# Optimization experiments

Measured on AMD Instinct MI355X. Metric: run time of the kernel, lower is better.

The kernel has to match this reference:

```python
import jax, jax.numpy as jnp
import numpy as np

N_NODES = 100000


def gcn_conv(x, edge_index, W, b, n_nodes):
    """PyG GCNConv: linear -> add self-loops -> symmetric-normalized scatter-sum -> bias."""
    h = x @ W  # [N, F_out]
    loop = jnp.arange(n_nodes, dtype=edge_index.dtype)
    src = jnp.concatenate([edge_index[0], loop])
    dst = jnp.concatenate([edge_index[1], loop])
    # degree of destination nodes (self-loops included)
    deg = jax.ops.segment_sum(jnp.ones_like(dst, dtype=h.dtype), dst, num_segments=n_nodes)
    dinv = jnp.where(deg > 0, jax.lax.rsqrt(deg), 0.0)
    norm = dinv[src] * dinv[dst]  # [E+N]
    msg = h[src] * norm[:, None]  # gather + scale
    out = jax.ops.segment_sum(msg, dst, num_segments=n_nodes)  # scatter-add
    return out + b


def setup_inputs() -> dict:
    key = jax.random.key(0)
    k1, k2, k3, k4 = jax.random.split(key, 4)
    d_in, hidden, out = 128, 256, 64
    x = jax.random.normal(k1, (N_NODES, d_in), dtype=jnp.float32)
    edge_index = jax.random.randint(k2, (2, 800000), 0, N_NODES, dtype=jnp.int64)
    W1 = jax.random.normal(k3, (d_in, hidden), dtype=jnp.float32) * (1.0 / np.sqrt(d_in))
    b1 = jnp.zeros((hidden,), dtype=jnp.float32)
    W2 = jax.random.normal(k4, (hidden, out), dtype=jnp.float32) * (1.0 / np.sqrt(hidden))
    b2 = jnp.zeros((out,), dtype=jnp.float32)
    return {"x": x, "edge_index": edge_index, "W1": W1, "b1": b1, "W2": W2, "b2": b2}


def reference(x, edge_index, W1, b1, W2, b2):
    h = jax.nn.relu(gcn_conv(x, edge_index, W1, b1, N_NODES))
    # dropout p=0 (module default) -> identity
    return gcn_conv(h, edge_index, W2, b2, N_NODES)
```

## Files before the change

kernel.cpp:

```cpp
#include <hip/hip_runtime.h>
#include <hip/hip_bf16.h>

#define N_NODES 100000
#define D_IN 128
#define HID 256
#define D_OUT 64
#define TR 32
#define NBUK 196
#define BSH 9
#define MGRID 625

typedef __attribute__((ext_vector_type(8))) short bf8;
typedef __attribute__((ext_vector_type(4))) float f4;

static __device__ __forceinline__ unsigned short f2bf(float f) {
    __hip_bfloat16 h = __float2bfloat16(f);
    return *reinterpret_cast<unsigned short*>(&h);
}
static __device__ __forceinline__ float bflo(unsigned int u) { return __uint_as_float(u << 16); }
static __device__ __forceinline__ float bfhi(unsigned int u) { return __uint_as_float(u & 0xffff0000u); }

static __device__ __forceinline__ void fma8(float* a, float w, uint4 u) {
    a[0] += w * bflo(u.x); a[1] += w * bfhi(u.x);
    a[2] += w * bflo(u.y); a[3] += w * bfhi(u.y);
    a[4] += w * bflo(u.z); a[5] += w * bfhi(u.z);
    a[6] += w * bflo(u.w); a[7] += w * bfhi(u.w);
}
static __device__ __forceinline__ void fma4(float* a, float w, uint2 u) {
    a[0] += w * bflo(u.x); a[1] += w * bfhi(u.x);
    a[2] += w * bflo(u.y); a[3] += w * bfhi(u.y);
}


__global__ __launch_bounds__(256) void k_prep(const float* __restrict__ x,
                                              unsigned long long* __restrict__ xb,
                                              const float* __restrict__ W1,
                                              unsigned short* __restrict__ W1t,
                                              const float* __restrict__ W2,
                                              unsigned short* __restrict__ W2t,
                                              const int* __restrict__ dst, int E,
                                              int* __restrict__ hist2d) {
    int b = blockIdx.x, t = threadIdx.x;
    if (b < 12500) {
        int i = b * 256 + t;
        float4 v = ((const float4*)x)[i];
        unsigned long long o = (unsigned long long)f2bf(v.x) |
                               ((unsigned long long)f2bf(v.y) << 16) |
                               ((unsigned long long)f2bf(v.z) << 32) |
                               ((unsigned long long)f2bf(v.w) << 48);
        xb[i] = o;
    } else if (b < 12628) {
        int i = (b - 12500) * 256 + t;
        int n = i >> 7, k = i & 127;
        W1t[i] = f2bf(W1[k * HID + n]);
    } else if (b < 12692) {
        int i = (b - 12628) * 256 + t;
        int n = i >> 8, k = i & 255;
        W2t[i] = f2bf(W2[k * D_OUT + n]);
    } else {
        int hb = b - 12692;
        __shared__ int h[NBUK];
        if (t < NBUK) h[t] = 0;
        __syncthreads();
        int base = hb * 4096;
        for (int j = 0; j < 16; j++) {
            int e = base + j * 256 + t;
            if (e < E) atomicAdd(&h[dst[e] >> BSH], 1);
        }
        __syncthreads();
        if (t < NBUK) hist2d[hb * NBUK + t] = h[t];
    }
}


__global__ __launch_bounds__(256) void k_scanB1(const int* __restrict__ hist2d,
                                                int* __restrict__ blockbase,
                                                int* __restrict__ bsumB, int nbb) {
    __shared__ int s[256];
    int u = blockIdx.x, t = threadIdx.x;
    int v = (t < nbb) ? hist2d[t * NBUK + u] : 0;
    s[t] = v;
    __syncthreads();
    for (int off = 1; off < 256; off <<= 1) {
        int w = (t >= off) ? s[t - off] : 0;
        __syncthreads();
        s[t] += w;
        __syncthreads();
    }
    if (t < nbb) blockbase[t * NBUK + u] = s[t] - v;
    if (t == 255) bsumB[u] = s[255];
}

static __device__ __forceinline__ void bucket_scan(const int* __restrict__ bsumB,
                                                   int* s, int* exs, int t) {
    int v = (t < NBUK) ? bsumB[t] : 0;
    s[t] = v;
    __syncthreads();
    for (int off = 1; off < 256; off <<= 1) {
        int w = (t >= off) ? s[t - off] : 0;
        __syncthreads();
        s[t] += w;
        __syncthreads();
    }
    if (t < NBUK) exs[t] = s[t] - v;
    if (t == NBUK - 1) exs[NBUK] = s[t];
    __syncthreads();
}


__global__ __launch_bounds__(256) void k_bin(const int* __restrict__ src,
                                             const int* __restrict__ dst, int E,
                                             const int* __restrict__ blockbase,
                                             const int* __restrict__ bsumB,
                                             unsigned int* __restrict__ bin) {
    __shared__ int s[256], exs[NBUK + 1];
    __shared__ int baseL[NBUK], rankL[NBUK];
    int t = threadIdx.x;
    bucket_scan(bsumB, s, exs, t);
    if (t < NBUK) {
        baseL[t] = exs[t] + blockbase[blockIdx.x * NBUK + t];
        rankL[t] = 0;
    }
    __syncthreads();
    int base = blockIdx.x * 4096;
    for (int j = 0; j < 16; j++) {
        int e = base + j * 256 + t;
        if (e < E) {
            int sv = src[e], d = dst[e];
            int bu = d >> BSH;
            int r = atomicAdd(&rankL[bu], 1);
            bin[baseL[bu] + r] = ((unsigned int)(d & 511) << 17) | (unsigned int)sv;
        }
    }
}


__global__ __launch_bounds__(256) void k_cntscan(const unsigned int* __restrict__ bin,
                                                 const int* __restrict__ bsumB,
                                                 int* __restrict__ row_ptr,
                                                 float* __restrict__ dinv) {
    __shared__ int sb[256], exs[NBUK + 1];
    __shared__ int c[512];
    __shared__ int s[256];
    int b = blockIdx.x, t = threadIdx.x;
    bucket_scan(bsumB, sb, exs, t);
    int lo = exs[b], hi = exs[b + 1];
    c[t] = 0;
    c[t + 256] = 0;
    __syncthreads();
    for (int e = lo + t; e < hi; e += 256) atomicAdd(&c[bin[e] >> 17], 1);
    __syncthreads();
    int a0 = c[2 * t], a1 = c[2 * t + 1];
    s[t] = a0 + a1;
    __syncthreads();
    for (int off = 1; off < 256; off <<= 1) {
        int u = (t >= off) ? s[t - off] : 0;
        __syncthreads();
        s[t] += u;
        __syncthreads();
    }
    int ex = (t > 0) ? s[t - 1] : 0;
    int n0 = (b << BSH) + 2 * t;
    if (n0 < N_NODES) {
        row_ptr[n0] = lo + ex;
        dinv[n0] = rsqrtf((float)a0 + 1.0f);
    }
    if (n0 + 1 < N_NODES) {
        row_ptr[n0 + 1] = lo + ex + a0;
        dinv[n0 + 1] = rsqrtf((float)a1 + 1.0f);
    }
    if (b == NBUK - 1 && t == 255) row_ptr[N_NODES] = exs[NBUK];
}


__global__ __launch_bounds__(256) void k_place(const unsigned int* __restrict__ bin,
                                               const int* __restrict__ bsumB,
                                               const int* __restrict__ row_ptr,
                                               const float* __restrict__ dinv,
                                               int2* __restrict__ cw) {
    __shared__ int sb[256], exs[NBUK + 1];
    __shared__ int cur[512];
    __shared__ float dl[512];
    int b = blockIdx.x, t = threadIdx.x;
    bucket_scan(bsumB, sb, exs, t);
    int node0 = b << BSH;
    int nbn = N_NODES - node0;
    if (nbn > 512) nbn = 512;
    if (t < nbn) {
        cur[t] = row_ptr[node0 + t];
        dl[t] = dinv[node0 + t];
    }
    if (t + 256 < nbn) {
        cur[t + 256] = row_ptr[node0 + t + 256];
        dl[t + 256] = dinv[node0 + t + 256];
    }
    __syncthreads();
    int lo = exs[b], hi = exs[b + 1];
    for (int e = lo + t; e < hi; e += 256) {
        unsigned int rec = bin[e];
        int sv = rec & 0x1FFFF;
        int dloc = rec >> 17;
        int pos = atomicAdd(&cur[dloc], 1);
        int2 v;
        v.x = sv;
        v.y = __float_as_int(dinv[sv] * dl[dloc]);
        cw[pos] = v;
    }
}


__global__ __launch_bounds__(256) void k_pull1(const int* __restrict__ row_ptr,
                                               const int2* __restrict__ cw,
                                               const uint4* __restrict__ xb4,
                                               const float* __restrict__ dinv,
                                               uint4* __restrict__ agg4) {
    int wave = (blockIdx.x * 256 + threadIdx.x) >> 6;
    int lane = threadIdx.x & 63;
    int g = lane >> 4, l = lane & 15;
    int node = wave * 4 + g;
    int beg = row_ptr[node], end = row_ptr[node + 1];
    float di = dinv[node];
    float a[8] = {0, 0, 0, 0, 0, 0, 0, 0};
    fma8(a, di * di, xb4[(size_t)node * 16 + l]);
    int e = beg;
    if (e + 4 <= end) {
        int2 c0 = cw[e], c1 = cw[e + 1], c2 = cw[e + 2], c3 = cw[e + 3];
        uint4 u0 = xb4[(size_t)c0.x * 16 + l];
        uint4 u1 = xb4[(size_t)c1.x * 16 + l];
        uint4 u2 = xb4[(size_t)c2.x * 16 + l];
        uint4 u3 = xb4[(size_t)c3.x * 16 + l];
        e += 4;
        for (; e + 4 <= end; e += 4) {
            int2 d0 = cw[e], d1 = cw[e + 1], d2 = cw[e + 2], d3 = cw[e + 3];
            uint4 v0 = xb4[(size_t)d0.x * 16 + l];
            uint4 v1 = xb4[(size_t)d1.x * 16 + l];
            uint4 v2 = xb4[(size_t)d2.x * 16 + l];
            uint4 v3 = xb4[(size_t)d3.x * 16 + l];
            fma8(a, __int_as_float(c0.y), u0);
            fma8(a, __int_as_float(c1.y), u1);
            fma8(a, __int_as_float(c2.y), u2);
            fma8(a, __int_as_float(c3.y), u3);
            c0 = d0; c1 = d1; c2 = d2; c3 = d3;
            u0 = v0; u1 = v1; u2 = v2; u3 = v3;
        }
        fma8(a, __int_as_float(c0.y), u0);
        fma8(a, __int_as_float(c1.y), u1);
        fma8(a, __int_as_float(c2.y), u2);
        fma8(a, __int_as_float(c3.y), u3);
    }
    for (; e < end; e++) {
        int2 c = cw[e];
        fma8(a, __int_as_float(c.y), xb4[(size_t)c.x * 16 + l]);
    }
    uint4 o;
    o.x = (unsigned int)f2bf(a[0]) | ((unsigned int)f2bf(a[1]) << 16);
    o.y = (unsigned int)f2bf(a[2]) | ((unsigned int)f2bf(a[3]) << 16);
    o.z = (unsigned int)f2bf(a[4]) | ((unsigned int)f2bf(a[5]) << 16);
    o.w = (unsigned int)f2bf(a[6]) | ((unsigned int)f2bf(a[7]) << 16);
    agg4[(size_t)node * 16 + l] = o;
}


__global__ __launch_bounds__(256) void k_fused_mfma(unsigned short* __restrict__ agg,
                                                    const unsigned short* __restrict__ W1t,
                                                    const float* __restrict__ b1,
                                                    const unsigned short* __restrict__ W2t) {
    __shared__ char sH[TR * HID * 2];
    int t = threadIdx.x, wave = t >> 6, lane = t & 63;
    int lr = lane & 15, lg = lane >> 4;

    bf8 w1f[4][4];
#pragma unroll
    for (int kk = 0; kk < 4; kk++)
#pragma unroll
        for (int tt = 0; tt < 4; tt++)
            w1f[kk][tt] = *(const bf8*)(W1t + (size_t)(wave * 64 + tt * 16 + lr) * D_IN + kk * 32 + lg * 8);
    bf8 w2f[8];
#pragma unroll
    for (int kk = 0; kk < 8; kk++)
        w2f[kk] = *(const bf8*)(W2t + (size_t)(wave * 16 + lr) * HID + kk * 32 + lg * 8);
    float bias[4];
#pragma unroll
    for (int tt = 0; tt < 4; tt++) bias[tt] = b1[wave * 64 + tt * 16 + lr];

    for (int it = 0; it < 5; it++) {
        size_t row0 = ((size_t)blockIdx.x + (size_t)it * MGRID) * TR;

        f4 acc1[4][2];
#pragma unroll
        for (int tt = 0; tt < 4; tt++)
#pragma unroll
            for (int h = 0; h < 2; h++) acc1[tt][h] = (f4){0.f, 0.f, 0.f, 0.f};

#pragma unroll
        for (int kk = 0; kk < 4; kk++) {
            bf8 a0 = *(const bf8*)(agg + (row0 + lr) * 128 + kk * 32 + lg * 8);
            bf8 a1 = *(const bf8*)(agg + (row0 + 16 + lr) * 128 + kk * 32 + lg * 8);
#pragma unroll
            for (int tt = 0; tt < 4; tt++) {
                acc1[tt][0] = __builtin_amdgcn_mfma_f32_16x16x32_bf16(a0, w1f[kk][tt], acc1[tt][0], 0, 0, 0);
                acc1[tt][1] = __builtin_amdgcn_mfma_f32_16x16x32_bf16(a1, w1f[kk][tt], acc1[tt][1], 0, 0, 0);
            }
        }

#pragma unroll
        for (int tt = 0; tt < 4; tt++) {
            int colc = wave * 64 + tt * 16 + lr;
#pragma unroll
            for (int h = 0; h < 2; h++) {
#pragma unroll
                for (int ri = 0; ri < 4; ri++) {
                    int row = h * 16 + lg * 4 + ri;
                    float hv = acc1[tt][h][ri] + bias[tt];
                    hv = hv > 0.f ? hv : 0.f;
                    *(unsigned short*)(sH + ((row * 512 + colc * 2) ^ ((row & 7) << 4))) = f2bf(hv);
                }
            }
        }
        __syncthreads();

        f4 acc2[2];
        acc2[0] = (f4){0.f, 0.f, 0.f, 0.f};
        acc2[1] = (f4){0.f, 0.f, 0.f, 0.f};
#pragma unroll
        for (int kk = 0; kk < 8; kk++) {
            bf8 a0 = *(const bf8*)(sH + ((lr * 512 + kk * 64 + lg * 16) ^ ((lr & 7) << 4)));
            bf8 a1 = *(const bf8*)(sH + (((16 + lr) * 512 + kk * 64 + lg * 16) ^ (((16 + lr) & 7) << 4)));
            acc2[0] = __builtin_amdgcn_mfma_f32_16x16x32_bf16(a0, w2f[kk], acc2[0], 0, 0, 0);
            acc2[1] = __builtin_amdgcn_mfma_f32_16x16x32_bf16(a1, w2f[kk], acc2[1], 0, 0, 0);
        }
        int colc = wave * 16 + lr;
#pragma unroll
        for (int h = 0; h < 2; h++)
#pragma unroll
            for (int ri = 0; ri < 4; ri++) {
                int row = h * 16 + lg * 4 + ri;
                agg[(row0 + row) * 128 + colc] = f2bf(acc2[h][ri]);
            }
        __syncthreads();
    }
}


__global__ __launch_bounds__(256) void k_pull2(const int* __restrict__ row_ptr,
                                               const int2* __restrict__ cw,
                                               const uint2* __restrict__ m2,
                                               const float* __restrict__ dinv,
                                               const float* __restrict__ b2,
                                               float4* __restrict__ out4) {
    int wave = (blockIdx.x * 256 + threadIdx.x) >> 6;
    int lane = threadIdx.x & 63;
    int g = lane >> 4, l = lane & 15;
    int node = wave * 4 + g;
    int beg = row_ptr[node], end = row_ptr[node + 1];
    float di = dinv[node];
    float a[4] = {0, 0, 0, 0};
    fma4(a, di * di, m2[(size_t)node * 32 + l]);
    int e = beg;
    if (e + 4 <= end) {
        int2 c0 = cw[e], c1 = cw[e + 1], c2 = cw[e + 2], c3 = cw[e + 3];
        uint2 u0 = m2[(size_t)c0.x * 32 + l];
        uint2 u1 = m2[(size_t)c1.x * 32 + l];
        uint2 u2 = m2[(size_t)c2.x * 32 + l];
        uint2 u3 = m2[(size_t)c3.x * 32 + l];
        e += 4;
        for (; e + 4 <= end; e += 4) {
            int2 d0 = cw[e], d1 = cw[e + 1], d2 = cw[e + 2], d3 = cw[e + 3];
            uint2 v0 = m2[(size_t)d0.x * 32 + l];
            uint2 v1 = m2[(size_t)d1.x * 32 + l];
            uint2 v2 = m2[(size_t)d2.x * 32 + l];
            uint2 v3 = m2[(size_t)d3.x * 32 + l];
            fma4(a, __int_as_float(c0.y), u0);
            fma4(a, __int_as_float(c1.y), u1);
            fma4(a, __int_as_float(c2.y), u2);
            fma4(a, __int_as_float(c3.y), u3);
            c0 = d0; c1 = d1; c2 = d2; c3 = d3;
            u0 = v0; u1 = v1; u2 = v2; u3 = v3;
        }
        fma4(a, __int_as_float(c0.y), u0);
        fma4(a, __int_as_float(c1.y), u1);
        fma4(a, __int_as_float(c2.y), u2);
        fma4(a, __int_as_float(c3.y), u3);
    }
    for (; e < end; e++) {
        int2 c = cw[e];
        fma4(a, __int_as_float(c.y), m2[(size_t)c.x * 32 + l]);
    }
    float4 bv = ((const float4*)b2)[l];
    float4 o;
    o.x = a[0] + bv.x;
    o.y = a[1] + bv.y;
    o.z = a[2] + bv.z;
    o.w = a[3] + bv.w;
    out4[(size_t)node * 16 + l] = o;
}


extern "C" void kernel_launch(void* const* d_in, const int* in_sizes, int n_in,
                              void* d_out, int out_size, void* d_ws, size_t ws_size,
                              hipStream_t stream) {
    const float* x  = (const float*)d_in[0];
    const int*   ei = (const int*)d_in[1];
    const float* W1 = (const float*)d_in[2];
    const float* b1 = (const float*)d_in[3];
    const float* W2 = (const float*)d_in[4];
    const float* b2 = (const float*)d_in[5];
    float* out = (float*)d_out;

    const int E = in_sizes[1] / 2;
    const int* src = ei;
    const int* dst = ei + E;

    char* ws = (char*)d_ws;
    int* row_ptr        = (int*)(ws + 0);
    int2* cw            = (int2*)(ws + 400640);
    float* dinv         = (float*)(ws + 6800640);
    unsigned short* W1t = (unsigned short*)(ws + 7201024);
    unsigned short* W2t = (unsigned short*)(ws + 7266560);
    unsigned short* xb  = (unsigned short*)(ws + 7299328);
    unsigned short* aggb = (unsigned short*)(ws + 32899328);
    unsigned int* bin   = (unsigned int*)aggb;
    int* hist2d         = (int*)((char*)aggb + 3200256);
    int* blockbase      = (int*)((char*)aggb + 3354112);
    int* bsumB          = (int*)((char*)aggb + 3507968);

    const int NBB = (E + 4095) / 4096;

    k_prep<<<12692 + NBB, 256, 0, stream>>>(x, (unsigned long long*)xb, W1, W1t, W2, W2t,
                                            dst, E, hist2d);
    k_scanB1<<<NBUK, 256, 0, stream>>>(hist2d, blockbase, bsumB, NBB);
    k_bin<<<NBB, 256, 0, stream>>>(src, dst, E, blockbase, bsumB, bin);
    k_cntscan<<<NBUK, 256, 0, stream>>>(bin, bsumB, row_ptr, dinv);
    k_place<<<NBUK, 256, 0, stream>>>(bin, bsumB, row_ptr, dinv, cw);
    k_pull1<<<6250, 256, 0, stream>>>(row_ptr, cw, (const uint4*)xb, dinv, (uint4*)aggb);
    k_fused_mfma<<<MGRID, 256, 0, stream>>>(aggb, W1t, b1, W2t);
    k_pull2<<<6250, 256, 0, stream>>>(row_ptr, cw, (const uint2*)aggb, dinv, b2, (float4*)out);
}
```

Baseline: 149.6 us.

## Assign one wave per node in pull kernels, splitting edges across four slots

Result: slower. 162.1 us (+8.4%).

```diff
diff --git a/kernel.cpp b/kernel.cpp
--- a/kernel.cpp
+++ b/kernel.cpp
@@ -214,50 +214,47 @@
                                                const uint4* __restrict__ xb4,
                                                const float* __restrict__ dinv,
                                                uint4* __restrict__ agg4) {
-    int wave = (blockIdx.x * 256 + threadIdx.x) >> 6;
+    int node = (blockIdx.x * 256 + threadIdx.x) >> 6;
     int lane = threadIdx.x & 63;
-    int g = lane >> 4, l = lane & 15;
-    int node = wave * 4 + g;
+    int slot = lane >> 4, l = lane & 15;
     int beg = row_ptr[node], end = row_ptr[node + 1];
     float di = dinv[node];
     float a[8] = {0, 0, 0, 0, 0, 0, 0, 0};
-    fma8(a, di * di, xb4[(size_t)node * 16 + l]);
-    int e = beg;
-    if (e + 4 <= end) {
-        int2 c0 = cw[e], c1 = cw[e + 1], c2 = cw[e + 2], c3 = cw[e + 3];
-        uint4 u0 = xb4[(size_t)c0.x * 16 + l];
-        uint4 u1 = xb4[(size_t)c1.x * 16 + l];
-        uint4 u2 = xb4[(size_t)c2.x * 16 + l];
-        uint4 u3 = xb4[(size_t)c3.x * 16 + l];
-        e += 4;
-        for (; e + 4 <= end; e += 4) {
-            int2 d0 = cw[e], d1 = cw[e + 1], d2 = cw[e + 2], d3 = cw[e + 3];
-            uint4 v0 = xb4[(size_t)d0.x * 16 + l];
-            uint4 v1 = xb4[(size_t)d1.x * 16 + l];
-            uint4 v2 = xb4[(size_t)d2.x * 16 + l];
-            uint4 v3 = xb4[(size_t)d3.x * 16 + l];
-            fma8(a, __int_as_float(c0.y), u0);
-            fma8(a, __int_as_float(c1.y), u1);
-            fma8(a, __int_as_float(c2.y), u2);
-            fma8(a, __int_as_float(c3.y), u3);
-            c0 = d0; c1 = d1; c2 = d2; c3 = d3;
-            u0 = v0; u1 = v1; u2 = v2; u3 = v3;
-        }
-        fma8(a, __int_as_float(c0.y), u0);
-        fma8(a, __int_as_float(c1.y), u1);
-        fma8(a, __int_as_float(c2.y), u2);
-        fma8(a, __int_as_float(c3.y), u3);
-    }
-    for (; e < end; e++) {
-        int2 c = cw[e];
-        fma8(a, __int_as_float(c.y), xb4[(size_t)c.x * 16 + l]);
-    }
-    uint4 o;
-    o.x = (unsigned int)f2bf(a[0]) | ((unsigned int)f2bf(a[1]) << 16);
-    o.y = (unsigned int)f2bf(a[2]) | ((unsigned int)f2bf(a[3]) << 16);
-    o.z = (unsigned int)f2bf(a[4]) | ((unsigned int)f2bf(a[5]) << 16);
-    o.w = (unsigned int)f2bf(a[6]) | ((unsigned int)f2bf(a[7]) << 16);
-    agg4[(size_t)node * 16 + l] = o;
+    float ws = (slot == 0) ? di * di : 0.f;
+    fma8(a, ws, xb4[(size_t)node * 16 + l]);
+    int deg = end - beg;
+    if (deg > 0) {
+        int nb = (deg + 3) >> 2;
+        int e = beg + slot;
+        bool valid = e < end;
+        int2 c = cw[valid ? e : beg];
+        float w = valid ? __int_as_float(c.y) : 0.f;
+        uint4 u = xb4[(size_t)c.x * 16 + l];
+        for (int it = 1; it < nb; it++) {
+            e += 4;
+            bool v2 = e < end;
+            int2 c2 = cw[v2 ? e : beg];
+            float nw = v2 ? __int_as_float(c2.y) : 0.f;
+            uint4 nu = xb4[(size_t)c2.x * 16 + l];
+            fma8(a, w, u);
+            w = nw;
+            u = nu;
+        }
+        fma8(a, w, u);
+    }
+#pragma unroll
+    for (int i = 0; i < 8; i++) {
+        a[i] += __shfl_xor(a[i], 16);
+        a[i] += __shfl_xor(a[i], 32);
+    }
+    if (slot == 0) {
+        uint4 o;
+        o.x = (unsigned int)f2bf(a[0]) | ((unsigned int)f2bf(a[1]) << 16);
+        o.y = (unsigned int)f2bf(a[2]) | ((unsigned int)f2bf(a[3]) << 16);
+        o.z = (unsigned int)f2bf(a[4]) | ((unsigned int)f2bf(a[5]) << 16);
+        o.w = (unsigned int)f2bf(a[6]) | ((unsigned int)f2bf(a[7]) << 16);
+        agg4[(size_t)node * 16 + l] = o;
+    }
 }
 
 
@@ -348,51 +345,48 @@
                                                const float* __restrict__ dinv,
                                                const float* __restrict__ b2,
                                                float4* __restrict__ out4) {
-    int wave = (blockIdx.x * 256 + threadIdx.x) >> 6;
+    int node = (blockIdx.x * 256 + threadIdx.x) >> 6;
     int lane = threadIdx.x & 63;
-    int g = lane >> 4, l = lane & 15;
-    int node = wave * 4 + g;
+    int slot = lane >> 4, l = lane & 15;
     int beg = row_ptr[node], end = row_ptr[node + 1];
     float di = dinv[node];
     float a[4] = {0, 0, 0, 0};
-    fma4(a, di * di, m2[(size_t)node * 32 + l]);
-    int e = beg;
-    if (e + 4 <= end) {
-        int2 c0 = cw[e], c1 = cw[e + 1], c2 = cw[e + 2], c3 = cw[e + 3];
-        uint2 u0 = m2[(size_t)c0.x * 32 + l];
-        uint2 u1 = m2[(size_t)c1.x * 32 + l];
-        uint2 u2 = m2[(size_t)c2.x * 32 + l];
-        uint2 u3 = m2[(size_t)c3.x * 32 + l];
-        e += 4;
-        for (; e + 4 <= end; e += 4) {
-            int2 d0 = cw[e], d1 = cw[e + 1], d2 = cw[e + 2], d3 = cw[e + 3];
-            uint2 v0 = m2[(size_t)d0.x * 32 + l];
-            uint2 v1 = m2[(size_t)d1.x * 32 + l];
-            uint2 v2 = m2[(size_t)d2.x * 32 + l];
-            uint2 v3 = m2[(size_t)d3.x * 32 + l];
-            fma4(a, __int_as_float(c0.y), u0);
-            fma4(a, __int_as_float(c1.y), u1);
-            fma4(a, __int_as_float(c2.y), u2);
-            fma4(a, __int_as_float(c3.y), u3);
-            c0 = d0; c1 = d1; c2 = d2; c3 = d3;
-            u0 = v0; u1 = v1; u2 = v2; u3 = v3;
-        }
-        fma4(a, __int_as_float(c0.y), u0);
-        fma4(a, __int_as_float(c1.y), u1);
-        fma4(a, __int_as_float(c2.y), u2);
-        fma4(a, __int_as_float(c3.y), u3);
-    }
-    for (; e < end; e++) {
-        int2 c = cw[e];
-        fma4(a, __int_as_float(c.y), m2[(size_t)c.x * 32 + l]);
-    }
-    float4 bv = ((const float4*)b2)[l];
-    float4 o;
-    o.x = a[0] + bv.x;
-    o.y = a[1] + bv.y;
-    o.z = a[2] + bv.z;
-    o.w = a[3] + bv.w;
-    out4[(size_t)node * 16 + l] = o;
+    float ws = (slot == 0) ? di * di : 0.f;
+    fma4(a, ws, m2[(size_t)node * 32 + l]);
+    int deg = end - beg;
+    if (deg > 0) {
+        int nb = (deg + 3) >> 2;
+        int e = beg + slot;
+        bool valid = e < end;
+        int2 c = cw[valid ? e : beg];
+        float w = valid ? __int_as_float(c.y) : 0.f;
+        uint2 u = m2[(size_t)c.x * 32 + l];
+        for (int it = 1; it < nb; it++) {
+            e += 4;
+            bool v2 = e < end;
+            int2 c2 = cw[v2 ? e : beg];
+            float nw = v2 ? __int_as_float(c2.y) : 0.f;
+            uint2 nu = m2[(size_t)c2.x * 32 + l];
+            fma4(a, w, u);
+            w = nw;
+            u = nu;
+        }
+        fma4(a, w, u);
+    }
+#pragma unroll
+    for (int i = 0; i < 4; i++) {
+        a[i] += __shfl_xor(a[i], 16);
+        a[i] += __shfl_xor(a[i], 32);
+    }
+    if (slot == 0) {
+        float4 bv = ((const float4*)b2)[l];
+        float4 o;
+        o.x = a[0] + bv.x;
+        o.y = a[1] + bv.y;
+        o.z = a[2] + bv.z;
+        o.w = a[3] + bv.w;
+        out4[(size_t)node * 16 + l] = o;
+    }
 }
 
 
@@ -432,7 +426,7 @@
     k_bin<<<NBB, 256, 0, stream>>>(src, dst, E, blockbase, bsumB, bin);
     k_cntscan<<<NBUK, 256, 0, stream>>>(bin, bsumB, row_ptr, dinv);
     k_place<<<NBUK, 256, 0, stream>>>(bin, bsumB, row_ptr, dinv, cw);
-    k_pull1<<<6250, 256, 0, stream>>>(row_ptr, cw, (const uint4*)xb, dinv, (uint4*)aggb);
+    k_pull1<<<25000, 256, 0, stream>>>(row_ptr, cw, (const uint4*)xb, dinv, (uint4*)aggb);
     k_fused_mfma<<<MGRID, 256, 0, stream>>>(aggb, W1t, b1, W2t);
-    k_pull2<<<6250, 256, 0, stream>>>(row_ptr, cw, (const uint2*)aggb, dinv, b2, (float4*)out);
-}
+    k_pull2<<<25000, 256, 0, stream>>>(row_ptr, cw, (const uint2*)aggb, dinv, b2, (float4*)out);
+}
```
